# Kernel tuning notes

Measured on AMD Instinct MI355X. Metric: run time of the kernel, lower is better.

The kernel has to match this reference:

```python
import jax, jax.numpy as jnp
import numpy as np

H = 256
H2 = H // 2
N = 1024
T = 12
B = 4


def setup_inputs() -> dict:
    key = jax.random.key(0)
    ks = jax.random.split(key, 12)
    s = lambda fan_in: 1.0 / np.sqrt(fan_in)
    inp = {
        "node_embeddings": jax.random.normal(ks[0], (B, N, H), jnp.float32),
        # origin encoder: Linear(H,H) -> ReLU -> Linear(H,H2)
        "W1o": jax.random.normal(ks[1], (H, H), jnp.float32) * s(H),
        "b1o": jnp.zeros((H,), jnp.float32),
        "W2o": jax.random.normal(ks[2], (H, H2), jnp.float32) * s(H),
        "b2o": jnp.zeros((H2,), jnp.float32),
        # dest encoder
        "W1d": jax.random.normal(ks[3], (H, H), jnp.float32) * s(H),
        "b1d": jnp.zeros((H,), jnp.float32),
        "W2d": jax.random.normal(ks[4], (H, H2), jnp.float32) * s(H),
        "b2d": jnp.zeros((H2,), jnp.float32),
        # bilinear: out = o @ Wb @ d^T + bb  (torch nn.Bilinear(H2,H2,1))
        "Wb": jax.random.normal(ks[5], (H2, H2), jnp.float32) * s(H2),
        "bb": jnp.zeros((), jnp.float32),
        # horizon predictor: Linear(1, T) -> ReLU
        "wh": jax.random.normal(ks[6], (T,), jnp.float32),
        "bh": jnp.zeros((T,), jnp.float32),
    }
    return inp


def reference(node_embeddings, W1o, b1o, W2o, b2o, W1d, b1d, W2d, b2d, Wb, bb, wh, bh):
    # encoders (dropout is identity at eval)
    o = jax.nn.relu(node_embeddings @ W1o + b1o) @ W2o + b2o      # (B,N,H2)
    d = jax.nn.relu(node_embeddings @ W1d + b1d) @ W2d + b2d      # (B,N,H2)
    # bilinear score without materializing (B,N,N,H2):
    oW = jnp.einsum("bik,kl->bil", o, Wb)                          # (B,N,H2)
    scores = jnp.einsum("bil,bjl->bij", oW, d) + bb                # (B,N,N)
    # horizon predictor Linear(1,T)+ReLU, then permute to (B,T,N,N)
    pred = jax.nn.relu(scores[..., None] * wh + bh)                # (B,N,N,T)
    pred = jnp.transpose(pred, (0, 3, 1, 2))                       # (B,T,N,N)
    return jax.nn.relu(pred)
```

## Files before the change

kernel.cpp:

```cpp
#include <hip/hip_runtime.h>
#include <hip/hip_bf16.h>

constexpr int H  = 256;
constexpr int H2 = 128;
constexpr int N  = 1024;
constexpr int T  = 12;
constexpr int B  = 4;
constexpr int M  = B * N;

using short8 = __attribute__((ext_vector_type(8))) short;
using f32x4  = __attribute__((ext_vector_type(4))) float;

__device__ __forceinline__ unsigned short f2bf(float f) {
    union { float f; unsigned int u; } v; v.f = f;
    unsigned int u = v.u;
    u += 0x7FFFu + ((u >> 16) & 1u);
    return (unsigned short)(u >> 16);
}

__global__ void prep_kernel(const float* __restrict__ x,
                            const float* __restrict__ W1o, const float* __restrict__ W1d,
                            const float* __restrict__ b1o, const float* __restrict__ b1d,
                            const float* __restrict__ W2o, const float* __restrict__ b2o,
                            const float* __restrict__ W2d, const float* __restrict__ b2d,
                            const float* __restrict__ Wb,
                            unsigned short* __restrict__ xb,
                            unsigned short* __restrict__ W1T,
                            unsigned short* __restrict__ W2T,
                            float* __restrict__ bias1, float* __restrict__ bias2)
{
    const int NX  = M * H;
    const int NW1 = 512 * H;
    const int NW2 = 256 * H;
    const int TOT = NX + NW1 + NW2 + 512 + 256;
    for (int i = blockIdx.x * blockDim.x + threadIdx.x; i < TOT;
         i += gridDim.x * blockDim.x) {
        if (i < NX) {
            xb[i] = f2bf(x[i]);
        } else if (i < NX + NW1) {
            const int j = i - NX, n = j >> 8, k = j & 255;
            const float v = (n < 256) ? W1o[k * H + n] : W1d[k * H + (n - 256)];
            W1T[j] = f2bf(v);
        } else if (i < NX + NW1 + NW2) {
            const int j = i - NX - NW1, n = j >> 8, k = j & 255;
            float v;
            if (n < 128) {
                float acc = 0.f;
#pragma unroll 8
                for (int l2 = 0; l2 < H2; ++l2)
                    acc = fmaf(W2o[k * H2 + l2], Wb[l2 * H2 + n], acc);
                v = acc;
            } else {
                v = W2d[k * H2 + (n - 128)];
            }
            W2T[j] = f2bf(v);
        } else if (i < NX + NW1 + NW2 + 512) {
            const int j = i - NX - NW1 - NW2;
            bias1[j] = (j < 256) ? b1o[j] : b1d[j - 256];
        } else {
            const int j = i - NX - NW1 - NW2 - 512;
            float v;
            if (j < 128) {
                float acc = 0.f;
#pragma unroll 8
                for (int l2 = 0; l2 < H2; ++l2)
                    acc = fmaf(b2o[l2], Wb[l2 * H2 + j], acc);
                v = acc;
            } else {
                v = b2d[j - 128];
            }
            bias2[j] = v;
        }
    }
}

template<bool RELU>
__device__ __forceinline__ void enc_body(
    const unsigned short* __restrict__ A, int lda,
    const unsigned short* __restrict__ Bt,
    const float* __restrict__ bias,
    unsigned short* __restrict__ C, int ldc)
{
    __shared__ unsigned short Abuf[64 * 40];
    __shared__ unsigned short Bbuf[64 * 40];
    const int tid = threadIdx.x;
    const int w  = tid >> 6;
    const int l  = tid & 63;
    const int lr = tid >> 2;
    const int lk = (tid & 3) * 8;

    uint4 aR = *(const uint4*)(A + (size_t)lr * lda + lk);
    uint4 bR = *(const uint4*)(Bt + (size_t)lr * 256 + lk);

    f32x4 z = {0.f, 0.f, 0.f, 0.f};
    f32x4 acc[4] = {z, z, z, z};

    for (int kc = 0; kc < 256; kc += 32) {
        if (kc) __syncthreads();
        *(uint4*)&Abuf[lr * 40 + lk] = aR;
        *(uint4*)&Bbuf[lr * 40 + lk] = bR;
        __syncthreads();
        if (kc + 32 < 256) {
            aR = *(const uint4*)(A + (size_t)lr * lda + kc + 32 + lk);
            bR = *(const uint4*)(Bt + (size_t)lr * 256 + kc + 32 + lk);
        }
        const int q8 = (l >> 4) * 8;
        const short8 bf = *(const short8*)&Bbuf[(w * 16 + (l & 15)) * 40 + q8];
#pragma unroll
        for (int it = 0; it < 4; ++it) {
            const short8 af = *(const short8*)&Abuf[(it * 16 + (l & 15)) * 40 + q8];
            acc[it] = __builtin_amdgcn_mfma_f32_16x16x32_bf16(af, bf, acc[it], 0, 0, 0);
        }
    }

    const int n  = w * 16 + (l & 15);
    const int r0 = (l >> 4) * 4;
    const float bn = bias[n];
#pragma unroll
    for (int it = 0; it < 4; ++it)
#pragma unroll
        for (int r = 0; r < 4; ++r) {
            float v = acc[it][r] + bn;
            if (RELU) v = fmaxf(v, 0.f);
            C[(size_t)(it * 16 + r0 + r) * ldc + n] = f2bf(v);
        }
}

__global__ __launch_bounds__(256) void enc1_kernel(
    const unsigned short* __restrict__ xb, const unsigned short* __restrict__ W1T,
    const float* __restrict__ bias1, unsigned short* __restrict__ h)
{
    const int bx = blockIdx.x, by = blockIdx.y;
    enc_body<true>(xb + (size_t)by * 64 * 256, 256,
                   W1T + (size_t)bx * 64 * 256,
                   bias1 + bx * 64,
                   h + (size_t)by * 64 * 512 + bx * 64, 512);
}

__global__ __launch_bounds__(256) void enc2_kernel(
    const unsigned short* __restrict__ h, const unsigned short* __restrict__ W2T,
    const float* __restrict__ bias2, unsigned short* __restrict__ od)
{
    const int bx = blockIdx.x, by = blockIdx.y;
    enc_body<false>(h + (size_t)by * 64 * 512 + (bx >> 1) * 256, 512,
                    W2T + (size_t)bx * 64 * 256,
                    bias2 + bx * 64,
                    od + (size_t)by * 64 * 256 + bx * 64, 256);
}

__global__ __launch_bounds__(256) void k3_kernel(
    const unsigned short* __restrict__ od,
    const float* __restrict__ bbp, const float* __restrict__ wh,
    const float* __restrict__ bh, float* __restrict__ out)
{
    __shared__ unsigned short Obuf[64 * 40];
    __shared__ unsigned short Dbuf[64 * 40];
    const int tid = threadIdx.x;
    const int w  = tid >> 6;
    const int l  = tid & 63;
    const int lr = tid >> 2;
    const int lk = (tid & 3) * 8;
    const int b  = blockIdx.z;
    const int i0 = blockIdx.y * 64;
    const int j0 = blockIdx.x * 64;
    const unsigned short* Ob = od + ((size_t)b * N + i0) * 256;
    const unsigned short* Db = od + ((size_t)b * N + j0) * 256 + 128;

    uint4 oR = *(const uint4*)(Ob + (size_t)lr * 256 + lk);
    uint4 dR = *(const uint4*)(Db + (size_t)lr * 256 + lk);

    f32x4 z = {0.f, 0.f, 0.f, 0.f};
    f32x4 acc[4] = {z, z, z, z};

    for (int kc = 0; kc < H2; kc += 32) {
        if (kc) __syncthreads();
        *(uint4*)&Obuf[lr * 40 + lk] = oR;
        *(uint4*)&Dbuf[lr * 40 + lk] = dR;
        __syncthreads();
        if (kc + 32 < H2) {
            oR = *(const uint4*)(Ob + (size_t)lr * 256 + kc + 32 + lk);
            dR = *(const uint4*)(Db + (size_t)lr * 256 + kc + 32 + lk);
        }
        const int q8 = (l >> 4) * 8;
        const short8 bf = *(const short8*)&Obuf[(w * 16 + (l & 15)) * 40 + q8];
#pragma unroll
        for (int it = 0; it < 4; ++it) {
            const short8 af = *(const short8*)&Dbuf[(it * 16 + (l & 15)) * 40 + q8];
            acc[it] = __builtin_amdgcn_mfma_f32_16x16x32_bf16(af, bf, acc[it], 0, 0, 0);
        }
    }

    const float bbv = bbp[0];
    float s[4][4];
#pragma unroll
    for (int it = 0; it < 4; ++it)
#pragma unroll
        for (int r = 0; r < 4; ++r) s[it][r] = acc[it][r] + bbv;

    const int iRow = i0 + w * 16 + (l & 15);
    const int r0   = (l >> 4) * 4;
#pragma unroll
    for (int t = 0; t < T; ++t) {
        const float wt = wh[t], bt = bh[t];
        float* ob = out + ((size_t)(b * T + t) * N + iRow) * N + j0 + r0;
#pragma unroll
        for (int it = 0; it < 4; ++it) {
            f32x4 v;
#pragma unroll
            for (int r = 0; r < 4; ++r)
                v[r] = fmaxf(fmaf(s[it][r], wt, bt), 0.f);
            *(f32x4*)(ob + it * 16) = v;
        }
    }
}

extern "C" void kernel_launch(void* const* d_in, const int* in_sizes, int n_in,
                              void* d_out, int out_size, void* d_ws, size_t ws_size,
                              hipStream_t stream) {
    const float* x   = (const float*)d_in[0];
    const float* W1o = (const float*)d_in[1];
    const float* b1o = (const float*)d_in[2];
    const float* W2o = (const float*)d_in[3];
    const float* b2o = (const float*)d_in[4];
    const float* W1d = (const float*)d_in[5];
    const float* b1d = (const float*)d_in[6];
    const float* W2d = (const float*)d_in[7];
    const float* b2d = (const float*)d_in[8];
    const float* Wb  = (const float*)d_in[9];
    const float* bb  = (const float*)d_in[10];
    const float* wh  = (const float*)d_in[11];
    const float* bh  = (const float*)d_in[12];
    float* out = (float*)d_out;

    float* bias1 = (float*)d_ws;
    float* bias2 = bias1 + 512;
    unsigned short* xb  = (unsigned short*)(bias2 + 256);
    unsigned short* W1T = xb + (size_t)M * H;
    unsigned short* W2T = W1T + 512 * H;
    unsigned short* h   = W2T + 256 * H;
    unsigned short* od  = h + (size_t)M * 512;

    prep_kernel<<<1024, 256, 0, stream>>>(x, W1o, W1d, b1o, b1d,
                                          W2o, b2o, W2d, b2d, Wb,
                                          xb, W1T, W2T, bias1, bias2);

    enc1_kernel<<<dim3(8, M / 64), 256, 0, stream>>>(xb, W1T, bias1, h);

    enc2_kernel<<<dim3(4, M / 64), 256, 0, stream>>>(h, W2T, bias2, od);

    k3_kernel<<<dim3(N / 64, N / 64, B), 256, 0, stream>>>(od, bb, wh, bh, out);
}
```

Baseline: 248.9 us.

## Fuse both encoder GEMMs into one kernel keeping hidden activations in LDS

The two encoder matmuls become a single kernel. Each block loads its 64-row slice of x once, computes the 512-wide hidden layer into shared memory, then runs the second layer from LDS, so the global round-trip of h and one launch are removed. The bilinear score kernel now stages the full K=128 O and D tiles into LDS with one barrier instead of looping over 32-wide chunks. The cost is much larger LDS use (about 132KB per block) and only 64 blocks for the encoder, which lowers occupancy and parallelism. Weight tiles are also loaded synchronously with no prefetch overlap.

```diff
diff --git a/kernel.cpp b/kernel.cpp
--- a/kernel.cpp
+++ b/kernel.cpp
@@ -74,78 +74,95 @@
     }
 }
 
-template<bool RELU>
-__device__ __forceinline__ void enc_body(
-    const unsigned short* __restrict__ A, int lda,
-    const unsigned short* __restrict__ Bt,
-    const float* __restrict__ bias,
-    unsigned short* __restrict__ C, int ldc)
+__global__ __launch_bounds__(256) void enc_fused_kernel(
+    const unsigned short* __restrict__ xb, const unsigned short* __restrict__ W1T,
+    const unsigned short* __restrict__ W2T,
+    const float* __restrict__ bias1, const float* __restrict__ bias2,
+    unsigned short* __restrict__ od)
 {
-    __shared__ unsigned short Abuf[64 * 40];
-    __shared__ unsigned short Bbuf[64 * 40];
+    __shared__ unsigned short Albs[64 * 264];
+    __shared__ unsigned short Bbuf[64 * 264];
+    __shared__ unsigned short Hbuf[64 * 520];
+
     const int tid = threadIdx.x;
-    const int w  = tid >> 6;
-    const int l  = tid & 63;
-    const int lr = tid >> 2;
-    const int lk = (tid & 3) * 8;
-
-    uint4 aR = *(const uint4*)(A + (size_t)lr * lda + lk);
-    uint4 bR = *(const uint4*)(Bt + (size_t)lr * 256 + lk);
-
-    f32x4 z = {0.f, 0.f, 0.f, 0.f};
-    f32x4 acc[4] = {z, z, z, z};
-
-    for (int kc = 0; kc < 256; kc += 32) {
-        if (kc) __syncthreads();
-        *(uint4*)&Abuf[lr * 40 + lk] = aR;
-        *(uint4*)&Bbuf[lr * 40 + lk] = bR;
+    const int w   = tid >> 6;
+    const int l   = tid & 63;
+    const int li  = l & 15;
+    const int q8  = (l >> 4) * 8;
+    const int r0  = (l >> 4) * 4;
+    const int lr  = tid >> 2;
+    const int lc  = (tid & 3) * 64;
+    const size_t row0 = (size_t)blockIdx.x * 64;
+
+    {
+        const unsigned short* src = xb + (row0 + lr) * 256 + lc;
+        unsigned short* dst = &Albs[lr * 264 + lc];
+#pragma unroll
+        for (int u = 0; u < 8; ++u)
+            *(uint4*)(dst + u * 8) = *(const uint4*)(src + u * 8);
+    }
+
+    for (int cx = 0; cx < 8; ++cx) {
+        {
+            const unsigned short* src = W1T + (size_t)(cx * 64 + lr) * 256 + lc;
+            unsigned short* dst = &Bbuf[lr * 264 + lc];
+#pragma unroll
+            for (int u = 0; u < 8; ++u)
+                *(uint4*)(dst + u * 8) = *(const uint4*)(src + u * 8);
+        }
         __syncthreads();
-        if (kc + 32 < 256) {
-            aR = *(const uint4*)(A + (size_t)lr * lda + kc + 32 + lk);
-            bR = *(const uint4*)(Bt + (size_t)lr * 256 + kc + 32 + lk);
-        }
-        const int q8 = (l >> 4) * 8;
-        const short8 bf = *(const short8*)&Bbuf[(w * 16 + (l & 15)) * 40 + q8];
-#pragma unroll
-        for (int it = 0; it < 4; ++it) {
-            const short8 af = *(const short8*)&Abuf[(it * 16 + (l & 15)) * 40 + q8];
-            acc[it] = __builtin_amdgcn_mfma_f32_16x16x32_bf16(af, bf, acc[it], 0, 0, 0);
-        }
-    }
-
-    const int n  = w * 16 + (l & 15);
-    const int r0 = (l >> 4) * 4;
-    const float bn = bias[n];
-#pragma unroll
-    for (int it = 0; it < 4; ++it)
-#pragma unroll
-        for (int r = 0; r < 4; ++r) {
-            float v = acc[it][r] + bn;
-            if (RELU) v = fmaxf(v, 0.f);
-            C[(size_t)(it * 16 + r0 + r) * ldc + n] = f2bf(v);
-        }
-}
-
-__global__ __launch_bounds__(256) void enc1_kernel(
-    const unsigned short* __restrict__ xb, const unsigned short* __restrict__ W1T,
-    const float* __restrict__ bias1, unsigned short* __restrict__ h)
-{
-    const int bx = blockIdx.x, by = blockIdx.y;
-    enc_body<true>(xb + (size_t)by * 64 * 256, 256,
-                   W1T + (size_t)bx * 64 * 256,
-                   bias1 + bx * 64,
-                   h + (size_t)by * 64 * 512 + bx * 64, 512);
-}
-
-__global__ __launch_bounds__(256) void enc2_kernel(
-    const unsigned short* __restrict__ h, const unsigned short* __restrict__ W2T,
-    const float* __restrict__ bias2, unsigned short* __restrict__ od)
-{
-    const int bx = blockIdx.x, by = blockIdx.y;
-    enc_body<false>(h + (size_t)by * 64 * 512 + (bx >> 1) * 256, 512,
-                    W2T + (size_t)bx * 64 * 256,
-                    bias2 + bx * 64,
-                    od + (size_t)by * 64 * 256 + bx * 64, 256);
+        f32x4 z = {0.f, 0.f, 0.f, 0.f};
+        f32x4 acc[4] = {z, z, z, z};
+#pragma unroll
+        for (int kc = 0; kc < 256; kc += 32) {
+            const short8 bf = *(const short8*)&Bbuf[(w * 16 + li) * 264 + kc + q8];
+#pragma unroll
+            for (int it = 0; it < 4; ++it) {
+                const short8 af = *(const short8*)&Albs[(it * 16 + li) * 264 + kc + q8];
+                acc[it] = __builtin_amdgcn_mfma_f32_16x16x32_bf16(af, bf, acc[it], 0, 0, 0);
+            }
+        }
+        const int col = cx * 64 + w * 16 + li;
+        const float bn = bias1[col];
+#pragma unroll
+        for (int it = 0; it < 4; ++it)
+#pragma unroll
+            for (int r = 0; r < 4; ++r)
+                Hbuf[(it * 16 + r0 + r) * 520 + col] =
+                    f2bf(fmaxf(acc[it][r] + bn, 0.f));
+        __syncthreads();
+    }
+
+    for (int dx = 0; dx < 4; ++dx) {
+        {
+            const unsigned short* src = W2T + (size_t)(dx * 64 + lr) * 256 + lc;
+            unsigned short* dst = &Bbuf[lr * 264 + lc];
+#pragma unroll
+            for (int u = 0; u < 8; ++u)
+                *(uint4*)(dst + u * 8) = *(const uint4*)(src + u * 8);
+        }
+        __syncthreads();
+        f32x4 z = {0.f, 0.f, 0.f, 0.f};
+        f32x4 acc[4] = {z, z, z, z};
+        const int abase = (dx >> 1) * 256;
+#pragma unroll
+        for (int kc = 0; kc < 256; kc += 32) {
+            const short8 bf = *(const short8*)&Bbuf[(w * 16 + li) * 264 + kc + q8];
+#pragma unroll
+            for (int it = 0; it < 4; ++it) {
+                const short8 af = *(const short8*)&Hbuf[(it * 16 + li) * 520 + abase + kc + q8];
+                acc[it] = __builtin_amdgcn_mfma_f32_16x16x32_bf16(af, bf, acc[it], 0, 0, 0);
+            }
+        }
+        const int ncol = dx * 64 + w * 16 + li;
+        const float bn = bias2[ncol];
+#pragma unroll
+        for (int it = 0; it < 4; ++it)
+#pragma unroll
+            for (int r = 0; r < 4; ++r)
+                od[(row0 + it * 16 + r0 + r) * 256 + ncol] = f2bf(acc[it][r] + bn);
+        if (dx < 3) __syncthreads();
+    }
 }
 
 __global__ __launch_bounds__(256) void k3_kernel(
@@ -153,39 +170,38 @@
     const float* __restrict__ bbp, const float* __restrict__ wh,
     const float* __restrict__ bh, float* __restrict__ out)
 {
-    __shared__ unsigned short Obuf[64 * 40];
-    __shared__ unsigned short Dbuf[64 * 40];
+    __shared__ unsigned short Obuf[64 * 136];
+    __shared__ unsigned short Dbuf[64 * 136];
     const int tid = threadIdx.x;
-    const int w  = tid >> 6;
-    const int l  = tid & 63;
-    const int lr = tid >> 2;
-    const int lk = (tid & 3) * 8;
-    const int b  = blockIdx.z;
-    const int i0 = blockIdx.y * 64;
-    const int j0 = blockIdx.x * 64;
+    const int w   = tid >> 6;
+    const int l   = tid & 63;
+    const int li  = l & 15;
+    const int q8  = (l >> 4) * 8;
+    const int lr  = tid >> 2;
+    const int lc  = (tid & 3) * 32;
+    const int b   = blockIdx.z;
+    const int i0  = blockIdx.y * 64;
+    const int j0  = blockIdx.x * 64;
     const unsigned short* Ob = od + ((size_t)b * N + i0) * 256;
     const unsigned short* Db = od + ((size_t)b * N + j0) * 256 + 128;
 
-    uint4 oR = *(const uint4*)(Ob + (size_t)lr * 256 + lk);
-    uint4 dR = *(const uint4*)(Db + (size_t)lr * 256 + lk);
+#pragma unroll
+    for (int u = 0; u < 4; ++u) {
+        *(uint4*)&Obuf[lr * 136 + lc + u * 8] =
+            *(const uint4*)(Ob + (size_t)lr * 256 + lc + u * 8);
+        *(uint4*)&Dbuf[lr * 136 + lc + u * 8] =
+            *(const uint4*)(Db + (size_t)lr * 256 + lc + u * 8);
+    }
+    __syncthreads();
 
     f32x4 z = {0.f, 0.f, 0.f, 0.f};
     f32x4 acc[4] = {z, z, z, z};
-
+#pragma unroll
     for (int kc = 0; kc < H2; kc += 32) {
-        if (kc) __syncthreads();
-        *(uint4*)&Obuf[lr * 40 + lk] = oR;
-        *(uint4*)&Dbuf[lr * 40 + lk] = dR;
-        __syncthreads();
-        if (kc + 32 < H2) {
-            oR = *(const uint4*)(Ob + (size_t)lr * 256 + kc + 32 + lk);
-            dR = *(const uint4*)(Db + (size_t)lr * 256 + kc + 32 + lk);
-        }
-        const int q8 = (l >> 4) * 8;
-        const short8 bf = *(const short8*)&Obuf[(w * 16 + (l & 15)) * 40 + q8];
+        const short8 bf = *(const short8*)&Obuf[(w * 16 + li) * 136 + kc + q8];
 #pragma unroll
         for (int it = 0; it < 4; ++it) {
-            const short8 af = *(const short8*)&Dbuf[(it * 16 + (l & 15)) * 40 + q8];
+            const short8 af = *(const short8*)&Dbuf[(it * 16 + li) * 136 + kc + q8];
             acc[it] = __builtin_amdgcn_mfma_f32_16x16x32_bf16(af, bf, acc[it], 0, 0, 0);
         }
     }
@@ -197,7 +213,7 @@
 #pragma unroll
         for (int r = 0; r < 4; ++r) s[it][r] = acc[it][r] + bbv;
 
-    const int iRow = i0 + w * 16 + (l & 15);
+    const int iRow = i0 + w * 16 + li;
     const int r0   = (l >> 4) * 4;
 #pragma unroll
     for (int t = 0; t < T; ++t) {
@@ -237,16 +253,13 @@
     unsigned short* xb  = (unsigned short*)(bias2 + 256);
     unsigned short* W1T = xb + (size_t)M * H;
     unsigned short* W2T = W1T + 512 * H;
-    unsigned short* h   = W2T + 256 * H;
-    unsigned short* od  = h + (size_t)M * 512;
+    unsigned short* od  = W2T + 256 * H;
 
     prep_kernel<<<1024, 256, 0, stream>>>(x, W1o, W1d, b1o, b1d,
                                           W2o, b2o, W2d, b2d, Wb,
                                           xb, W1T, W2T, bias1, bias2);
 
-    enc1_kernel<<<dim3(8, M / 64), 256, 0, stream>>>(xb, W1T, bias1, h);
-
-    enc2_kernel<<<dim3(4, M / 64), 256, 0, stream>>>(h, W2T, bias2, od);
+    enc_fused_kernel<<<M / 64, 256, 0, stream>>>(xb, W1T, W2T, bias1, bias2, od);
 
     k3_kernel<<<dim3(N / 64, N / 64, B), 256, 0, stream>>>(od, bb, wh, bh, out);
 }
```

Result: slower. 265.1 us (+6.5%).
